# Kernel tuning notes

Measured on AMD Instinct MI355X. Metric: run time of the kernel, lower is better.

Reference implementation:

```python
import jax, jax.numpy as jnp
import numpy as np

B, S, IN_C, OUT_C = 2, 1024, 4096, 32000


def setup_inputs() -> dict:
    key = jax.random.key(0)
    k1, k2, k3 = jax.random.split(key, 3)
    hidden_states = jax.random.normal(k1, (B, S, IN_C), dtype=jnp.float32)
    weight = jax.random.normal(k2, (OUT_C, IN_C), dtype=jnp.float32) * 0.02
    bias = jax.random.normal(k3, (OUT_C,), dtype=jnp.float32) * 0.02
    return {"hidden_states": hidden_states, "weight": weight, "bias": bias,
            "split_num": 2}


def reference(hidden_states, weight, bias, split_num):
    # SlicedLMHead: split in_features into `split_num` contiguous slices,
    # run each slice as a linear to outC, accumulate, then add bias.
    in_c = hidden_states.shape[-1]
    split_size = in_c // split_num // 2 * 2
    logits = None
    for i in range(split_num):
        start = i * split_size
        end = (i + 1) * split_size if i < split_num - 1 else in_c
        h_slice = hidden_states[:, :, start:end]          # [B, S, slice]
        w_slice = weight[:, start:end]                    # [outC, slice]
        logits_slice = jnp.einsum('bsc,vc->bsv', h_slice, w_slice)
        logits = logits_slice if logits is None else logits + logits_slice
    return logits + bias
```

## Files before the change

### kernel.cpp

```cpp
#include <hip/hip_runtime.h>
#include <hip/hip_bf16.h>


typedef __attribute__((ext_vector_type(8))) short bhalf8;
typedef __attribute__((ext_vector_type(4))) float f32x4;
typedef __attribute__((ext_vector_type(8))) unsigned short us8;

#define M_DIM 2048
#define N_DIM 32000
#define K_DIM 4096
#define BM 256
#define BN 256
#define BK 64
#define NT (K_DIM / BK)
#define MBLKS (M_DIM / BM)
#define NBLKS (N_DIM / BN)
#define NWG (MBLKS * NBLKS)

#define W_ELEMS ((size_t)N_DIM * K_DIM)
#define H_ELEMS ((size_t)M_DIM * K_DIM)
#define WS_NEEDED ((W_ELEMS + H_ELEMS) * 2)

#define GLOAD_LDS16(g, l) \
    __builtin_amdgcn_global_load_lds( \
        (const __attribute__((address_space(1))) unsigned int*)(g), \
        (__attribute__((address_space(3))) unsigned int*)(l), 16, 0, 0)

__device__ __forceinline__ unsigned short f2bf_rn(float f) {
    unsigned int u = __float_as_uint(f);
    u += 0x7FFFu + ((u >> 16) & 1u);
    return (unsigned short)(u >> 16);
}

__global__ __launch_bounds__(256)
void cvt_f32_bf16(const float* __restrict__ in, unsigned short* __restrict__ out,
                  size_t n8) {
    size_t i = (size_t)blockIdx.x * blockDim.x + threadIdx.x;
    const size_t stride = (size_t)gridDim.x * blockDim.x;
    for (; i < n8; i += stride) {
        const float4 v0 = ((const float4*)in)[i * 2];
        const float4 v1 = ((const float4*)in)[i * 2 + 1];
        us8 p;
        p[0] = f2bf_rn(v0.x); p[1] = f2bf_rn(v0.y);
        p[2] = f2bf_rn(v0.z); p[3] = f2bf_rn(v0.w);
        p[4] = f2bf_rn(v1.x); p[5] = f2bf_rn(v1.y);
        p[6] = f2bf_rn(v1.z); p[7] = f2bf_rn(v1.w);
        ((us8*)out)[i] = p;
    }
}

__global__ __launch_bounds__(512, 2)
void lmhead_gemm_256(const unsigned short* __restrict__ A,
                     const unsigned short* __restrict__ W,
                     const float* __restrict__ bias,
                     float* __restrict__ C)
{
    __shared__ unsigned short lds[65536];

    const int tid  = threadIdx.x;
    const int bid  = blockIdx.x;
    const int wgid = (bid & 7) * (NWG / 8) + (bid >> 3);
    const int mblk = wgid & (MBLKS - 1);
    const int nblk = wgid >> 3;

    const int lane = tid & 63;
    const int wv   = tid >> 6;
    const int wr   = wv >> 2;
    const int wc   = wv & 3;
    const int l15  = lane & 15;
    const int l4   = lane >> 4;

    const int strow = tid >> 3;
    const int sgsw  = ((tid & 7) ^ (strow & 7)) << 3;
    const unsigned short* const srcA = A + (size_t)(mblk * BM + strow) * K_DIM + sgsw;
    const unsigned short* const srcB = W + (size_t)(nblk * BN + strow) * K_DIM + sgsw;
    const int dstw = (tid & 448) * 8;

#define STAGE_A(u, h, BUF) { \
        const unsigned short* s_ = srcA + (size_t)((h) * 128) * K_DIM + (size_t)(u) * BK; \
        unsigned short* d_ = &lds[(((BUF) * 2 + (h)) * 8192) + dstw]; \
        GLOAD_LDS16(s_, d_); GLOAD_LDS16(s_ + (size_t)64 * K_DIM, d_ + 4096); }
#define STAGE_B(u, h, BUF) { \
        const unsigned short* s_ = srcB + (size_t)((h) * 128) * K_DIM + (size_t)(u) * BK; \
        unsigned short* d_ = &lds[32768 + (((BUF) * 2 + (h)) * 8192) + dstw]; \
        GLOAD_LDS16(s_, d_); GLOAD_LDS16(s_ + (size_t)64 * K_DIM, d_ + 4096); }
#define STAGE_TILE(u, BUF) { \
        STAGE_A(u, 0, BUF); STAGE_A(u, 1, BUF); \
        STAGE_B(u, 0, BUF); STAGE_B(u, 1, BUF); }

    const int swz0 = (l4 ^ (l15 & 7)) << 3;
    const int swz1 = ((4 + l4) ^ (l15 & 7)) << 3;
    const int arow = l15 * 64;
    const int brow = ((wc & 1) * 64 + l15) * 64;

    f32x4 acc[8][4] = {};
    bhalf8 af0[8], bf0[4];
    bhalf8 af1[8], bf1[4];

#define ISSUE_FRAGS(av, bv, BUF, SWZ) { \
        const unsigned short* _as = &lds[((BUF) * 2 + wr) * 8192]; \
        const unsigned short* _bs = &lds[32768 + ((BUF) * 2 + (wc >> 1)) * 8192]; \
        _Pragma("unroll") \
        for (int i = 0; i < 4; ++i) av[i]     = *(const bhalf8*)&_as[arow + (SWZ) + i * 1024]; \
        _Pragma("unroll") \
        for (int i = 0; i < 4; ++i) av[4 + i] = *(const bhalf8*)&_as[arow + (SWZ) + 4096 + i * 1024]; \
        _Pragma("unroll") \
        for (int j = 0; j < 4; ++j) bv[j]     = *(const bhalf8*)&_bs[brow + (SWZ) + j * 1024]; }

#define MFMA32(av, bv) { \
        _Pragma("unroll") \
        for (int i = 0; i < 8; ++i) \
            _Pragma("unroll") \
            for (int j = 0; j < 4; ++j) \
                acc[i][j] = __builtin_amdgcn_mfma_f32_16x16x32_bf16(av[i], bv[j], acc[i][j], 0, 0, 0); }

    STAGE_TILE(0, 0);
    STAGE_TILE(1, 1);
    asm volatile("s_waitcnt vmcnt(8)" ::: "memory");
    __builtin_amdgcn_sched_barrier(0);
    __builtin_amdgcn_s_barrier();
    ISSUE_FRAGS(af0, bf0, 0, swz0);

    #pragma unroll 1
    for (int t = 0; t < NT; ++t) {
        const int b = t & 1;

        ISSUE_FRAGS(af1, bf1, b, swz1);
        __builtin_amdgcn_sched_barrier(0);
        asm volatile("s_waitcnt lgkmcnt(12)" ::: "memory");
        __builtin_amdgcn_sched_barrier(0);
        __builtin_amdgcn_s_setprio(1);
        MFMA32(af0, bf0);
        __builtin_amdgcn_s_setprio(0);
        __builtin_amdgcn_sched_barrier(0);
        asm volatile("s_waitcnt lgkmcnt(0)" ::: "memory");
        __builtin_amdgcn_sched_barrier(0);
        __builtin_amdgcn_s_barrier();

        if (t + 2 < NT) STAGE_TILE(t + 2, b);
        __builtin_amdgcn_sched_barrier(0);
        if (t + 2 < NT) { asm volatile("s_waitcnt vmcnt(8)" ::: "memory"); }
        else            { asm volatile("s_waitcnt vmcnt(0)" ::: "memory"); }
        __builtin_amdgcn_sched_barrier(0);
        __builtin_amdgcn_s_barrier();
        if (t + 1 < NT) ISSUE_FRAGS(af0, bf0, b ^ 1, swz0);
        __builtin_amdgcn_sched_barrier(0);
        __builtin_amdgcn_s_setprio(1);
        MFMA32(af1, bf1);
        __builtin_amdgcn_s_setprio(0);
    }

    const size_t crow0 = (size_t)(mblk * BM + wr * 128 + l4 * 4);
    const int    ccol0 = nblk * BN + wc * 64 + l15;
    #pragma unroll
    for (int j = 0; j < 4; ++j) {
        const float bv = bias[ccol0 + j * 16];
        #pragma unroll
        for (int i = 0; i < 8; ++i) {
            const size_t base = (crow0 + (size_t)i * 16) * N_DIM + ccol0 + j * 16;
            #pragma unroll
            for (int r = 0; r < 4; ++r)
                C[base + (size_t)r * N_DIM] = acc[i][j][r] + bv;
        }
    }
#undef STAGE_A
#undef STAGE_B
#undef STAGE_TILE
#undef ISSUE_FRAGS
#undef MFMA32
}

__global__ __launch_bounds__(256, 2)
void lmhead_gemm_f32(const float* __restrict__ A, const float* __restrict__ W,
                     const float* __restrict__ bias, float* __restrict__ C) {
    __shared__ unsigned short As[2][128 * 64];
    __shared__ unsigned short Bs[2][128 * 64];

    const int tid  = threadIdx.x;
    const int bid  = blockIdx.x;
    const int mblk = bid & 15;
    const int nblk = bid >> 4;
    const int st_row = tid >> 3;
    const int st_g   = tid & 7;
    const int lane = tid & 63;
    const int wv   = tid >> 6;
    const int wm   = (wv >> 1) << 6;
    const int wn   = (wv & 1) << 6;
    const int l15  = lane & 15;
    const int l4   = lane >> 4;

    const float* aptr = A + (size_t)(mblk * 128 + st_row) * K_DIM + st_g * 8;
    const float* bptr = W + (size_t)(nblk * 128 + st_row) * K_DIM + st_g * 8;

    f32x4 acc[4][4] = {};
    float4 ra[4][2], rb[4][2];

    #pragma unroll
    for (int s = 0; s < 4; ++s) {
        const float* ap = aptr + (size_t)(s * 32) * K_DIM;
        const float* bp = bptr + (size_t)(s * 32) * K_DIM;
        ra[s][0] = *(const float4*)(ap);   ra[s][1] = *(const float4*)(ap + 4);
        rb[s][0] = *(const float4*)(bp);   rb[s][1] = *(const float4*)(bp + 4);
    }
    #pragma unroll
    for (int s = 0; s < 4; ++s) {
        const int row = s * 32 + st_row;
        const int off = row * 64 + ((st_g ^ (row & 7)) << 3);
        us8 pa, pb;
        #pragma unroll
        for (int j = 0; j < 4; ++j) {
            pa[j] = f2bf_rn(((const float*)&ra[s][0])[j]);
            pa[j + 4] = f2bf_rn(((const float*)&ra[s][1])[j]);
            pb[j] = f2bf_rn(((const float*)&rb[s][0])[j]);
            pb[j + 4] = f2bf_rn(((const float*)&rb[s][1])[j]);
        }
        *(us8*)&As[0][off] = pa;  *(us8*)&Bs[0][off] = pb;
    }
    __syncthreads();

    for (int t = 0; t < 64; ++t) {
        const int cur = t & 1;
        const bool more = (t + 1) < 64;
        if (more) {
            const float* ap = aptr + (size_t)(t + 1) * 64;
            const float* bp = bptr + (size_t)(t + 1) * 64;
            #pragma unroll
            for (int s = 0; s < 4; ++s) {
                ra[s][0] = *(const float4*)(ap + (size_t)(s * 32) * K_DIM);
                ra[s][1] = *(const float4*)(ap + (size_t)(s * 32) * K_DIM + 4);
                rb[s][0] = *(const float4*)(bp + (size_t)(s * 32) * K_DIM);
                rb[s][1] = *(const float4*)(bp + (size_t)(s * 32) * K_DIM + 4);
            }
        }
        const unsigned short* as = As[cur];
        const unsigned short* bs = Bs[cur];
        #pragma unroll
        for (int kk = 0; kk < 2; ++kk) {
            bhalf8 af[4], bfv[4];
            #pragma unroll
            for (int mf = 0; mf < 4; ++mf) {
                const int row = wm + mf * 16 + l15;
                af[mf] = *(const bhalf8*)&as[row * 64 + ((((kk << 2) + l4) ^ (row & 7)) << 3)];
            }
            #pragma unroll
            for (int nf = 0; nf < 4; ++nf) {
                const int row = wn + nf * 16 + l15;
                bfv[nf] = *(const bhalf8*)&bs[row * 64 + ((((kk << 2) + l4) ^ (row & 7)) << 3)];
            }
            #pragma unroll
            for (int mf = 0; mf < 4; ++mf)
                #pragma unroll
                for (int nf = 0; nf < 4; ++nf)
                    acc[mf][nf] = __builtin_amdgcn_mfma_f32_16x16x32_bf16(
                        af[mf], bfv[nf], acc[mf][nf], 0, 0, 0);
        }
        if (more) {
            const int nbuf = cur ^ 1;
            #pragma unroll
            for (int s = 0; s < 4; ++s) {
                const int row = s * 32 + st_row;
                const int off = row * 64 + ((st_g ^ (row & 7)) << 3);
                us8 pa, pb;
                #pragma unroll
                for (int j = 0; j < 4; ++j) {
                    pa[j] = f2bf_rn(((const float*)&ra[s][0])[j]);
                    pa[j + 4] = f2bf_rn(((const float*)&ra[s][1])[j]);
                    pb[j] = f2bf_rn(((const float*)&rb[s][0])[j]);
                    pb[j + 4] = f2bf_rn(((const float*)&rb[s][1])[j]);
                }
                *(us8*)&As[nbuf][off] = pa;  *(us8*)&Bs[nbuf][off] = pb;
            }
        }
        __syncthreads();
    }

    const size_t crow0 = (size_t)(mblk * 128 + wm + l4 * 4);
    const int    ccol0 = nblk * 128 + wn + l15;
    #pragma unroll
    for (int nf = 0; nf < 4; ++nf) {
        const float bv = bias[ccol0 + nf * 16];
        #pragma unroll
        for (int mf = 0; mf < 4; ++mf) {
            const size_t base = (crow0 + (size_t)mf * 16) * N_DIM + ccol0 + nf * 16;
            #pragma unroll
            for (int r = 0; r < 4; ++r)
                C[base + (size_t)r * N_DIM] = acc[mf][nf][r] + bv;
        }
    }
}

extern "C" void kernel_launch(void* const* d_in, const int* in_sizes, int n_in,
                              void* d_out, int out_size, void* d_ws, size_t ws_size,
                              hipStream_t stream) {
    const float* h = (const float*)d_in[0];
    const float* w = (const float*)d_in[1];
    const float* b = (const float*)d_in[2];
    float* out = (float*)d_out;

    if (ws_size >= WS_NEEDED) {
        unsigned short* wbf = (unsigned short*)d_ws;
        unsigned short* hbf = wbf + W_ELEMS;
        cvt_f32_bf16<<<2048, 256, 0, stream>>>(w, wbf, W_ELEMS / 8);
        cvt_f32_bf16<<<512, 256, 0, stream>>>(h, hbf, H_ELEMS / 8);
        lmhead_gemm_256<<<NWG, 512, 0, stream>>>(hbf, wbf, b, out);
    } else {
        lmhead_gemm_f32<<<4000, 256, 0, stream>>>(h, w, b, out);
    }
}
```

Measured before the change: 669.5 us.

## Pre-swizzle weights into MFMA fragment layout and load B directly from global

The weight conversion kernel now writes bf16 weights in a per-wave MFMA fragment order, so the GEMM can load B fragments straight from global memory into registers instead of staging them through LDS. LDS now holds only the A tile (halved footprint), and the main loop is restructured into half-K steps, interleaving register B loads with A LDS staging and MFMA issue. This removes LDS traffic and bank pressure for B, at the cost of more global-load latency exposed per wave. The pipeline depth for A also drops from two tiles ahead to one.

```diff
diff --git a/kernel.cpp b/kernel.cpp
--- a/kernel.cpp
+++ b/kernel.cpp
@@ -49,13 +49,39 @@
     }
 }
 
+__global__ __launch_bounds__(256)
+void cvt_w_frag(const float* __restrict__ w, unsigned short* __restrict__ wn) {
+    const int lane  = threadIdx.x & 63;
+    const int nwav  = gridDim.x * 4;
+    const int l15   = lane & 15;
+    const int l4g   = (lane >> 4) * 8;
+    for (int c = blockIdx.x * 4 + (threadIdx.x >> 6); c < 256000; c += nwav) {
+        const int j  = c & 3;
+        const int kk = (c >> 2) & 1;
+        const int t  = (c >> 3) & 63;
+        const int wc = (c >> 9) & 3;
+        const int nb = c >> 11;
+        const int row = nb * 256 + wc * 64 + j * 16 + l15;
+        const int k   = t * 64 + kk * 32 + l4g;
+        const float* s = w + (size_t)row * K_DIM + k;
+        const float4 v0 = *(const float4*)s;
+        const float4 v1 = *(const float4*)(s + 4);
+        us8 p;
+        p[0] = f2bf_rn(v0.x); p[1] = f2bf_rn(v0.y);
+        p[2] = f2bf_rn(v0.z); p[3] = f2bf_rn(v0.w);
+        p[4] = f2bf_rn(v1.x); p[5] = f2bf_rn(v1.y);
+        p[6] = f2bf_rn(v1.z); p[7] = f2bf_rn(v1.w);
+        *(us8*)(wn + (size_t)c * 512 + lane * 8) = p;
+    }
+}
+
 __global__ __launch_bounds__(512, 2)
-void lmhead_gemm_256(const unsigned short* __restrict__ A,
-                     const unsigned short* __restrict__ W,
+void lmhead_gemm_bd2(const unsigned short* __restrict__ A,
+                     const unsigned short* __restrict__ Wn,
                      const float* __restrict__ bias,
                      float* __restrict__ C)
 {
-    __shared__ unsigned short lds[65536];
+    __shared__ unsigned short lds[32768];
 
     const int tid  = threadIdx.x;
     const int bid  = blockIdx.x;
@@ -73,81 +99,97 @@
     const int strow = tid >> 3;
     const int sgsw  = ((tid & 7) ^ (strow & 7)) << 3;
     const unsigned short* const srcA = A + (size_t)(mblk * BM + strow) * K_DIM + sgsw;
-    const unsigned short* const srcB = W + (size_t)(nblk * BN + strow) * K_DIM + sgsw;
     const int dstw = (tid & 448) * 8;
 
 #define STAGE_A(u, h, BUF) { \
         const unsigned short* s_ = srcA + (size_t)((h) * 128) * K_DIM + (size_t)(u) * BK; \
         unsigned short* d_ = &lds[(((BUF) * 2 + (h)) * 8192) + dstw]; \
         GLOAD_LDS16(s_, d_); GLOAD_LDS16(s_ + (size_t)64 * K_DIM, d_ + 4096); }
-#define STAGE_B(u, h, BUF) { \
-        const unsigned short* s_ = srcB + (size_t)((h) * 128) * K_DIM + (size_t)(u) * BK; \
-        unsigned short* d_ = &lds[32768 + (((BUF) * 2 + (h)) * 8192) + dstw]; \
-        GLOAD_LDS16(s_, d_); GLOAD_LDS16(s_ + (size_t)64 * K_DIM, d_ + 4096); }
-#define STAGE_TILE(u, BUF) { \
-        STAGE_A(u, 0, BUF); STAGE_A(u, 1, BUF); \
-        STAGE_B(u, 0, BUF); STAGE_B(u, 1, BUF); }
+#define STAGE_AT(u, BUF) { STAGE_A(u, 0, BUF); STAGE_A(u, 1, BUF); }
 
     const int swz0 = (l4 ^ (l15 & 7)) << 3;
     const int swz1 = ((4 + l4) ^ (l15 & 7)) << 3;
     const int arow = l15 * 64;
-    const int brow = ((wc & 1) * 64 + l15) * 64;
-
-    f32x4 acc[8][4] = {};
-    bhalf8 af0[8], bf0[4];
-    bhalf8 af1[8], bf1[4];
-
-#define ISSUE_FRAGS(av, bv, BUF, SWZ) { \
+
+#define ISSUE_AFK(DST, BUF, SWZ) { \
         const unsigned short* _as = &lds[((BUF) * 2 + wr) * 8192]; \
-        const unsigned short* _bs = &lds[32768 + ((BUF) * 2 + (wc >> 1)) * 8192]; \
-        _Pragma("unroll") \
-        for (int i = 0; i < 4; ++i) av[i]     = *(const bhalf8*)&_as[arow + (SWZ) + i * 1024]; \
-        _Pragma("unroll") \
-        for (int i = 0; i < 4; ++i) av[4 + i] = *(const bhalf8*)&_as[arow + (SWZ) + 4096 + i * 1024]; \
-        _Pragma("unroll") \
-        for (int j = 0; j < 4; ++j) bv[j]     = *(const bhalf8*)&_bs[brow + (SWZ) + j * 1024]; }
-
-#define MFMA32(av, bv) { \
         _Pragma("unroll") \
         for (int i = 0; i < 8; ++i) \
+            DST[i] = *(const bhalf8*)&_as[arow + (SWZ) + i * 1024]; }
+
+    const unsigned short* const wbase =
+        Wn + (size_t)(nblk * 4 + wc) * 262144 + lane * 8;
+
+#define BLOADK(DST, T, KK) { \
+        _Pragma("unroll") \
+        for (int j = 0; j < 4; ++j) \
+            DST[j] = *(const bhalf8*)(wbase + ((size_t)((T) * 2 + (KK)) * 4 + j) * 512); }
+
+    f32x4 acc[8][4] = {};
+    bhalf8 afk0[8], afk1[8];
+    bhalf8 bgk0[4], bgk1[4];
+
+#define MFMA16Q(AF, BASE, BG) { \
+        _Pragma("unroll") \
+        for (int i = 0; i < 4; ++i) \
             _Pragma("unroll") \
             for (int j = 0; j < 4; ++j) \
-                acc[i][j] = __builtin_amdgcn_mfma_f32_16x16x32_bf16(av[i], bv[j], acc[i][j], 0, 0, 0); }
-
-    STAGE_TILE(0, 0);
-    STAGE_TILE(1, 1);
-    asm volatile("s_waitcnt vmcnt(8)" ::: "memory");
-    __builtin_amdgcn_sched_barrier(0);
+                acc[(BASE) + i][j] = __builtin_amdgcn_mfma_f32_16x16x32_bf16( \
+                    AF[(BASE) + i], BG[j], acc[(BASE) + i][j], 0, 0, 0); }
+
+#define SBAR __builtin_amdgcn_sched_barrier(0)
+
+    STAGE_AT(0, 0);
+    SBAR;
+    BLOADK(bgk0, 0, 0);
+    SBAR;
+    asm volatile("s_waitcnt vmcnt(4)" ::: "memory");
+    SBAR;
     __builtin_amdgcn_s_barrier();
-    ISSUE_FRAGS(af0, bf0, 0, swz0);
+    ISSUE_AFK(afk0, 0, swz0);
 
     #pragma unroll 1
     for (int t = 0; t < NT; ++t) {
         const int b = t & 1;
-
-        ISSUE_FRAGS(af1, bf1, b, swz1);
-        __builtin_amdgcn_sched_barrier(0);
-        asm volatile("s_waitcnt lgkmcnt(12)" ::: "memory");
-        __builtin_amdgcn_sched_barrier(0);
+        const bool more = (t + 1) < NT;
+
+        asm volatile("s_waitcnt vmcnt(0)" ::: "memory");
+        SBAR;
+        asm volatile("s_waitcnt lgkmcnt(0)" ::: "memory");
+        SBAR;
+        BLOADK(bgk1, t, 1);
+        SBAR;
+        if (more) STAGE_AT(t + 1, b ^ 1);
+        SBAR;
+        ISSUE_AFK(afk1, b, swz1);
+        SBAR;
         __builtin_amdgcn_s_setprio(1);
-        MFMA32(af0, bf0);
+        MFMA16Q(afk0, 0, bgk0);
         __builtin_amdgcn_s_setprio(0);
-        __builtin_amdgcn_sched_barrier(0);
+        __builtin_amdgcn_s_setprio(1);
+        MFMA16Q(afk0, 4, bgk0);
+        __builtin_amdgcn_s_setprio(0);
+        SBAR;
         asm volatile("s_waitcnt lgkmcnt(0)" ::: "memory");
-        __builtin_amdgcn_sched_barrier(0);
+        SBAR;
+        if (more) { asm volatile("s_waitcnt vmcnt(4)" ::: "memory"); }
+        else      { asm volatile("s_waitcnt vmcnt(0)" ::: "memory"); }
+        SBAR;
+        if (more) BLOADK(bgk0, t + 1, 0);
+        SBAR;
+        __builtin_amdgcn_s_setprio(1);
+        MFMA16Q(afk1, 0, bgk1);
+        __builtin_amdgcn_s_setprio(0);
+        __builtin_amdgcn_s_setprio(1);
+        MFMA16Q(afk1, 4, bgk1);
+        __builtin_amdgcn_s_setprio(0);
+        SBAR;
+        if (more) { asm volatile("s_waitcnt vmcnt(4)" ::: "memory"); }
+        else      { asm volatile("s_waitcnt vmcnt(0)" ::: "memory"); }
+        SBAR;
         __builtin_amdgcn_s_barrier();
-
-        if (t + 2 < NT) STAGE_TILE(t + 2, b);
-        __builtin_amdgcn_sched_barrier(0);
-        if (t + 2 < NT) { asm volatile("s_waitcnt vmcnt(8)" ::: "memory"); }
-        else            { asm volatile("s_waitcnt vmcnt(0)" ::: "memory"); }
-        __builtin_amdgcn_sched_barrier(0);
-        __builtin_amdgcn_s_barrier();
-        if (t + 1 < NT) ISSUE_FRAGS(af0, bf0, b ^ 1, swz0);
-        __builtin_amdgcn_sched_barrier(0);
-        __builtin_amdgcn_s_setprio(1);
-        MFMA32(af1, bf1);
-        __builtin_amdgcn_s_setprio(0);
+        if (more) ISSUE_AFK(afk0, b ^ 1, swz0);
+        SBAR;
     }
 
     const size_t crow0 = (size_t)(mblk * BM + wr * 128 + l4 * 4);
@@ -164,10 +206,11 @@
         }
     }
 #undef STAGE_A
-#undef STAGE_B
-#undef STAGE_TILE
-#undef ISSUE_FRAGS
-#undef MFMA32
+#undef STAGE_AT
+#undef ISSUE_AFK
+#undef BLOADK
+#undef MFMA16Q
+#undef SBAR
 }
 
 __global__ __launch_bounds__(256, 2)
@@ -300,9 +343,9 @@
     if (ws_size >= WS_NEEDED) {
         unsigned short* wbf = (unsigned short*)d_ws;
         unsigned short* hbf = wbf + W_ELEMS;
-        cvt_f32_bf16<<<2048, 256, 0, stream>>>(w, wbf, W_ELEMS / 8);
+        cvt_w_frag<<<2048, 256, 0, stream>>>(w, wbf);
         cvt_f32_bf16<<<512, 256, 0, stream>>>(h, hbf, H_ELEMS / 8);
-        lmhead_gemm_256<<<NWG, 512, 0, stream>>>(hbf, wbf, b, out);
+        lmhead_gemm_bd2<<<NWG, 512, 0, stream>>>(hbf, wbf, b, out);
     } else {
         lmhead_gemm_f32<<<4000, 256, 0, stream>>>(h, w, b, out);
     }
```

Result: slower. 745.5 us (+11.3%).

## Restructure bf16 GEMM main loop into 8-phase quarter-tile pipeline

Applied to the files above, without the earlier changes.

Replaces the two-phase per-K-tile loop with an eight-phase schedule over pairs of K tiles. Each phase issues part of the LDS fragment reads and part of the global-to-LDS staging, then runs a quarter of the MFMA block, with barriers and waitcnts between phases. The aim is to interleave memory traffic with matrix math at finer grain and cut fragment register pressure. In exchange there are many more workgroup barriers and a much more delicate buffer-reuse ordering, which raises correctness and stall risk.

```diff
diff --git a/kernel.cpp b/kernel.cpp
--- a/kernel.cpp
+++ b/kernel.cpp
@@ -84,9 +84,6 @@
         const unsigned short* s_ = srcB + (size_t)((h) * 128) * K_DIM + (size_t)(u) * BK; \
         unsigned short* d_ = &lds[32768 + (((BUF) * 2 + (h)) * 8192) + dstw]; \
         GLOAD_LDS16(s_, d_); GLOAD_LDS16(s_ + (size_t)64 * K_DIM, d_ + 4096); }
-#define STAGE_TILE(u, BUF) { \
-        STAGE_A(u, 0, BUF); STAGE_A(u, 1, BUF); \
-        STAGE_B(u, 0, BUF); STAGE_B(u, 1, BUF); }
 
     const int swz0 = (l4 ^ (l15 & 7)) << 3;
     const int swz1 = ((4 + l4) ^ (l15 & 7)) << 3;
@@ -94,60 +91,111 @@
     const int brow = ((wc & 1) * 64 + l15) * 64;
 
     f32x4 acc[8][4] = {};
-    bhalf8 af0[8], bf0[4];
-    bhalf8 af1[8], bf1[4];
-
-#define ISSUE_FRAGS(av, bv, BUF, SWZ) { \
+    bhalf8 af0[4][2], af1[4][2], bf01[2][2], bf23[2][2];
+
+#define READ_AF0(BUF) { \
         const unsigned short* _as = &lds[((BUF) * 2 + wr) * 8192]; \
+        _Pragma("unroll") \
+        for (int i = 0; i < 4; ++i) { \
+            af0[i][0] = *(const bhalf8*)&_as[arow + swz0 + i * 1024]; \
+            af0[i][1] = *(const bhalf8*)&_as[arow + swz1 + i * 1024]; } }
+#define READ_AF1(BUF) { \
+        const unsigned short* _as = &lds[((BUF) * 2 + wr) * 8192]; \
+        _Pragma("unroll") \
+        for (int i = 0; i < 4; ++i) { \
+            af1[i][0] = *(const bhalf8*)&_as[arow + swz0 + 4096 + i * 1024]; \
+            af1[i][1] = *(const bhalf8*)&_as[arow + swz1 + 4096 + i * 1024]; } }
+#define READ_BF01(BUF) { \
         const unsigned short* _bs = &lds[32768 + ((BUF) * 2 + (wc >> 1)) * 8192]; \
         _Pragma("unroll") \
-        for (int i = 0; i < 4; ++i) av[i]     = *(const bhalf8*)&_as[arow + (SWZ) + i * 1024]; \
-        _Pragma("unroll") \
-        for (int i = 0; i < 4; ++i) av[4 + i] = *(const bhalf8*)&_as[arow + (SWZ) + 4096 + i * 1024]; \
-        _Pragma("unroll") \
-        for (int j = 0; j < 4; ++j) bv[j]     = *(const bhalf8*)&_bs[brow + (SWZ) + j * 1024]; }
-
-#define MFMA32(av, bv) { \
-        _Pragma("unroll") \
-        for (int i = 0; i < 8; ++i) \
+        for (int j = 0; j < 2; ++j) { \
+            bf01[j][0] = *(const bhalf8*)&_bs[brow + swz0 + j * 1024]; \
+            bf01[j][1] = *(const bhalf8*)&_bs[brow + swz1 + j * 1024]; } }
+#define READ_BF23(BUF) { \
+        const unsigned short* _bs = &lds[32768 + ((BUF) * 2 + (wc >> 1)) * 8192]; \
+        _Pragma("unroll") \
+        for (int j = 0; j < 2; ++j) { \
+            bf23[j][0] = *(const bhalf8*)&_bs[brow + swz0 + (2 + j) * 1024]; \
+            bf23[j][1] = *(const bhalf8*)&_bs[brow + swz1 + (2 + j) * 1024]; } }
+
+#define MFMA8Q(AF, BF, IOFF, JOFF) { \
+        _Pragma("unroll") \
+        for (int i = 0; i < 4; ++i) \
             _Pragma("unroll") \
-            for (int j = 0; j < 4; ++j) \
-                acc[i][j] = __builtin_amdgcn_mfma_f32_16x16x32_bf16(av[i], bv[j], acc[i][j], 0, 0, 0); }
-
-    STAGE_TILE(0, 0);
-    STAGE_TILE(1, 1);
-    asm volatile("s_waitcnt vmcnt(8)" ::: "memory");
-    __builtin_amdgcn_sched_barrier(0);
-    __builtin_amdgcn_s_barrier();
-    ISSUE_FRAGS(af0, bf0, 0, swz0);
+            for (int j = 0; j < 2; ++j) \
+                _Pragma("unroll") \
+                for (int kk = 0; kk < 2; ++kk) \
+                    acc[(IOFF) + i][(JOFF) + j] = __builtin_amdgcn_mfma_f32_16x16x32_bf16( \
+                        AF[i][kk], BF[j][kk], acc[(IOFF) + i][(JOFF) + j], 0, 0, 0); }
+
+#define SBAR  __builtin_amdgcn_sched_barrier(0)
+#define BARR  __builtin_amdgcn_s_barrier()
+#define LGKM(n) asm volatile("s_waitcnt lgkmcnt(" #n ")" ::: "memory")
+#define VMC(n)  asm volatile("s_waitcnt vmcnt(" #n ")" ::: "memory")
+#define PRIO1 __builtin_amdgcn_s_setprio(1)
+#define PRIO0 __builtin_amdgcn_s_setprio(0)
+
+    STAGE_A(0, 0, 0); STAGE_A(0, 1, 0);
+    STAGE_B(0, 0, 0); STAGE_B(0, 1, 0);
+    STAGE_B(1, 0, 1); STAGE_B(1, 1, 1);
+    SBAR;
+    VMC(4);
+    SBAR;
+    BARR;
+    READ_AF0(0); READ_BF01(0);
+    SBAR;
 
     #pragma unroll 1
-    for (int t = 0; t < NT; ++t) {
-        const int b = t & 1;
-
-        ISSUE_FRAGS(af1, bf1, b, swz1);
-        __builtin_amdgcn_sched_barrier(0);
-        asm volatile("s_waitcnt lgkmcnt(12)" ::: "memory");
-        __builtin_amdgcn_sched_barrier(0);
-        __builtin_amdgcn_s_setprio(1);
-        MFMA32(af0, bf0);
-        __builtin_amdgcn_s_setprio(0);
-        __builtin_amdgcn_sched_barrier(0);
-        asm volatile("s_waitcnt lgkmcnt(0)" ::: "memory");
-        __builtin_amdgcn_sched_barrier(0);
-        __builtin_amdgcn_s_barrier();
-
-        if (t + 2 < NT) STAGE_TILE(t + 2, b);
-        __builtin_amdgcn_sched_barrier(0);
-        if (t + 2 < NT) { asm volatile("s_waitcnt vmcnt(8)" ::: "memory"); }
-        else            { asm volatile("s_waitcnt vmcnt(0)" ::: "memory"); }
-        __builtin_amdgcn_sched_barrier(0);
-        __builtin_amdgcn_s_barrier();
-        if (t + 1 < NT) ISSUE_FRAGS(af0, bf0, b ^ 1, swz0);
-        __builtin_amdgcn_sched_barrier(0);
-        __builtin_amdgcn_s_setprio(1);
-        MFMA32(af1, bf1);
-        __builtin_amdgcn_s_setprio(0);
+    for (int s2 = 0; s2 < NT; s2 += 2) {
+        const int T1 = s2 + 1;
+        const bool m2 = (s2 + 2) < NT;
+
+        READ_BF23(0); STAGE_A(T1, 0, 1); SBAR;
+        BARR; LGKM(4); SBAR;
+        PRIO1; MFMA8Q(af0, bf01, 0, 0); PRIO0; SBAR;
+        BARR;
+        READ_AF1(0); STAGE_A(T1, 1, 1); SBAR;
+        BARR; LGKM(8); SBAR;
+        PRIO1; MFMA8Q(af0, bf23, 0, 2); PRIO0; SBAR;
+        BARR;
+        if (m2) STAGE_B(s2 + 2, 0, 0);
+        SBAR;
+        BARR; LGKM(0); SBAR;
+        PRIO1; MFMA8Q(af1, bf01, 4, 0); PRIO0; SBAR;
+        if (m2) { VMC(2); } else { VMC(0); }
+        SBAR;
+        BARR;
+        READ_AF0(1); READ_BF01(1);
+        if (m2) STAGE_B(s2 + 2, 1, 0);
+        SBAR;
+        BARR; SBAR;
+        PRIO1; MFMA8Q(af1, bf23, 4, 2); PRIO0; SBAR;
+        BARR;
+        READ_BF23(1);
+        if (m2) STAGE_A(s2 + 2, 0, 0);
+        SBAR;
+        BARR; LGKM(4); SBAR;
+        PRIO1; MFMA8Q(af0, bf01, 0, 0); PRIO0; SBAR;
+        BARR;
+        READ_AF1(1);
+        if (m2) STAGE_A(s2 + 2, 1, 0);
+        SBAR;
+        BARR; LGKM(8); SBAR;
+        PRIO1; MFMA8Q(af0, bf23, 0, 2); PRIO0; SBAR;
+        BARR;
+        if (m2) STAGE_B(T1 + 2, 0, 1);
+        SBAR;
+        BARR; LGKM(0); SBAR;
+        PRIO1; MFMA8Q(af1, bf01, 4, 0); PRIO0; SBAR;
+        if (m2) { VMC(2); } else { VMC(0); }
+        SBAR;
+        BARR;
+        if (m2) { READ_AF0(0); READ_BF01(0); }
+        if (m2) STAGE_B(T1 + 2, 1, 1);
+        SBAR;
+        BARR; SBAR;
+        PRIO1; MFMA8Q(af1, bf23, 4, 2); PRIO0; SBAR;
+        BARR;
     }
 
     const size_t crow0 = (size_t)(mblk * BM + wr * 128 + l4 * 4);
@@ -165,9 +213,17 @@
     }
 #undef STAGE_A
 #undef STAGE_B
-#undef STAGE_TILE
-#undef ISSUE_FRAGS
-#undef MFMA32
+#undef READ_AF0
+#undef READ_AF1
+#undef READ_BF01
+#undef READ_BF23
+#undef MFMA8Q
+#undef SBAR
+#undef BARR
+#undef LGKM
+#undef VMC
+#undef PRIO1
+#undef PRIO0
 }
 
 __global__ __launch_bounds__(256, 2)
```

Result: faster. 622.3 us (-7.1%).
